# Kernel optimization log

Hardware: AMD Instinct MI355X
Metric: run time of the kernel (lower is better)

The kernel has to match this reference:

```python
import jax, jax.numpy as jnp
import numpy as np

B, S, D, H = 4, 2048, 1024, 16
HD = D // H  # 64


def setup_inputs() -> dict:
    key = jax.random.key(0)
    ks = jax.random.split(key, 9)
    s = 1.0 / np.sqrt(D)
    return {
        "x": jax.random.normal(ks[0], (B, S, D), dtype=jnp.float32),
        "Wq": jax.random.normal(ks[1], (D, D), dtype=jnp.float32) * s,
        "bq": jax.random.normal(ks[2], (D,), dtype=jnp.float32) * 0.01,
        "Wk": jax.random.normal(ks[3], (D, D), dtype=jnp.float32) * s,
        "bk": jax.random.normal(ks[4], (D,), dtype=jnp.float32) * 0.01,
        "Wv": jax.random.normal(ks[5], (D, D), dtype=jnp.float32) * s,
        "bv": jax.random.normal(ks[6], (D,), dtype=jnp.float32) * 0.01,
        "Wo": jax.random.normal(ks[7], (D, D), dtype=jnp.float32) * s,
        "bo": jax.random.normal(ks[8], (D,), dtype=jnp.float32) * 0.01,
    }


def reference(x, Wq, bq, Wk, bk, Wv, bv, Wo, bo):
    b, s, _ = x.shape
    # projections -> [b, h, s, hd]
    def proj(W, bias):
        return (x @ W.T + bias).reshape(b, s, H, HD).transpose(0, 2, 1, 3)
    q, k, v = proj(Wq, bq), proj(Wk, bk), proj(Wv, bv)
    # NOTE: source multiplies by sqrt(head_dim)**0.5 = head_dim**0.25 (quirk kept)
    scale = jnp.asarray(HD, dtype=x.dtype) ** 0.25
    scores = jnp.einsum("bhqd,bhkd->bhqk", q, k) * scale
    causal = jnp.tril(jnp.ones((s, s), dtype=bool))
    scores = jnp.where(causal, scores, -jnp.inf)
    attn = jax.nn.softmax(scores, axis=-1)  # dropout p=0 (eval) -> identity
    out = jnp.einsum("bhqk,bhkd->bhqd", attn, v)
    out = out.transpose(0, 2, 1, 3).reshape(b, s, D)
    return out @ Wo.T + bo
```

## Files before the change

### kernel.cpp

```cpp
#include <hip/hip_runtime.h>
#include <hip/hip_fp16.h>


typedef unsigned short u16;
typedef unsigned int u32;
typedef _Float16 half8 __attribute__((ext_vector_type(8)));
typedef float f32x4 __attribute__((ext_vector_type(4)));
typedef unsigned short ushort8 __attribute__((ext_vector_type(8)));
typedef unsigned short us4 __attribute__((ext_vector_type(4)));
typedef unsigned int u32x2 __attribute__((ext_vector_type(2)));

#define SCL2 4.0816663172343815f
#define SWZ(r) ((((r) ^ ((r) >> 3))) & 7)

__device__ __forceinline__ u16 f2h(float f) {
  return __half_as_ushort(__float2half(f));
}

__device__ __forceinline__ us4 pack4(float a, float b, float c, float d) {
  u32x2 t;
  t[0] = __builtin_bit_cast(u32, __builtin_amdgcn_cvt_pkrtz(a, b));
  t[1] = __builtin_bit_cast(u32, __builtin_amdgcn_cvt_pkrtz(c, d));
  return __builtin_bit_cast(us4, t);
}

__device__ __forceinline__ void gload16(const void* gsrc, void* ldst) {
  typedef __attribute__((address_space(1))) const void glob_t;
  typedef __attribute__((address_space(3))) void lds_t;
  __builtin_amdgcn_global_load_lds((glob_t*)gsrc, (lds_t*)ldst, 16, 0, 0);
}

__device__ __forceinline__ f32x4 mfma_f16(half8 a, half8 b, f32x4 c) {
  return __builtin_amdgcn_mfma_f32_16x16x32_f16(a, b, c, 0, 0, 0);
}

__global__ __launch_bounds__(256) void cvt_f32_f16(const float* __restrict__ in,
                                                   u16* __restrict__ out, int n8) {
  int i = blockIdx.x * 256 + threadIdx.x;
  if (i >= n8) return;
  const float4* p = (const float4*)in + (size_t)i * 2;
  float4 a = p[0], b = p[1];
  ushort8 v;
  v[0] = f2h(a.x); v[1] = f2h(a.y); v[2] = f2h(a.z); v[3] = f2h(a.w);
  v[4] = f2h(b.x); v[5] = f2h(b.y); v[6] = f2h(b.z); v[7] = f2h(b.w);
  *(ushort8*)(out + (size_t)i * 8) = v;
}

__device__ __forceinline__ void gemm_body(const u16* __restrict__ A, const u16* __restrict__ Bw,
                                          const float* __restrict__ bias,
                                          u16* __restrict__ Ch, float* __restrict__ Cf,
                                          u16* __restrict__ Vtp) {
  __shared__ __align__(16) u16 sA[128 * 32];
  __shared__ __align__(16) u16 sB[128 * 32];
  const int m0 = blockIdx.y * 128, n0 = blockIdx.x * 128;
  const int tid = threadIdx.x, w = tid >> 6, l = tid & 63;
  const int wm = (w >> 1) * 64, wn = (w & 1) * 64;
  f32x4 acc[4][4] = {};
  const int srow = tid >> 2, sch = (tid & 3) * 8;
  char* sAb = (char*)sA + w * 1024;
  char* sBb = (char*)sB + w * 1024;
  const u16* Ag0 = A + (size_t)(m0 + srow) * 1024 + sch;
  const u16* Ag1 = A + (size_t)(m0 + 64 + srow) * 1024 + sch;
  const u16* Bg0 = Bw + (size_t)(n0 + srow) * 1024 + sch;
  const u16* Bg1 = Bw + (size_t)(n0 + 64 + srow) * 1024 + sch;
  for (int kt = 0; kt < 32; ++kt) {
    const int k0 = kt * 32;
    __syncthreads();
    gload16(Ag0 + k0, sAb);
    gload16(Ag1 + k0, sAb + 4096);
    gload16(Bg0 + k0, sBb);
    gload16(Bg1 + k0, sBb + 4096);
    __syncthreads();
    half8 a[4], b[4];
#pragma unroll
    for (int mf = 0; mf < 4; ++mf)
      a[mf] = *(const half8*)&sA[(wm + mf * 16 + (l & 15)) * 32 + (l >> 4) * 8];
#pragma unroll
    for (int nf = 0; nf < 4; ++nf)
      b[nf] = *(const half8*)&sB[(wn + nf * 16 + (l & 15)) * 32 + (l >> 4) * 8];
#pragma unroll
    for (int mf = 0; mf < 4; ++mf)
#pragma unroll
      for (int nf = 0; nf < 4; ++nf)
        acc[mf][nf] = mfma_f16(a[mf], b[nf], acc[mf][nf]);
  }
  if (Vtp) {
#pragma unroll
    for (int nf = 0; nf < 4; ++nf) {
      const int col = n0 + wn + nf * 16 + (l & 15);
      const float bv = bias[col];
#pragma unroll
      for (int mf = 0; mf < 4; ++mf) {
        const int row = m0 + wm + mf * 16 + (l >> 4) * 4;
        us4 v;
#pragma unroll
        for (int r = 0; r < 4; ++r) v[r] = f2h(acc[mf][nf][r] + bv);
        *(us4*)(Vtp + (size_t)((row >> 11) * 16 + (col >> 6)) * 131072 +
                (size_t)(col & 63) * 2048 + (row & 2047)) = v;
      }
    }
  } else {
#pragma unroll
    for (int nf = 0; nf < 4; ++nf) {
      const int col = n0 + wn + nf * 16 + (l & 15);
      const float bv = bias[col];
#pragma unroll
      for (int mf = 0; mf < 4; ++mf) {
#pragma unroll
        for (int r = 0; r < 4; ++r) {
          const int row = m0 + wm + mf * 16 + (l >> 4) * 4 + r;
          float v = acc[mf][nf][r] + bv;
          if (Cf) Cf[(size_t)row * 1024 + col] = v;
          else    Ch[(size_t)row * 1024 + col] = f2h(v);
        }
      }
    }
  }
}

struct QkvArgs {
  const u16* B[3];
  const float* bias[3];
  u16* C[3];
};

__global__ __launch_bounds__(256) void gemm_qkv(const u16* __restrict__ A, QkvArgs ga) {
  const int z = blockIdx.z;
  if (z == 2) gemm_body(A, ga.B[2], ga.bias[2], nullptr, nullptr, ga.C[2]);
  else        gemm_body(A, ga.B[z], ga.bias[z], ga.C[z], nullptr, nullptr);
}

__global__ __launch_bounds__(256) void gemm_out(const u16* __restrict__ A, const u16* __restrict__ Bw,
                                                const float* __restrict__ bias, float* __restrict__ C) {
  gemm_body(A, Bw, bias, nullptr, C, nullptr);
}

__global__ __launch_bounds__(256) void attn_fused(const u16* __restrict__ Qb, const u16* __restrict__ Kb,
                                                  const u16* __restrict__ Vt, u16* __restrict__ Ob) {
  __shared__ __align__(16) u16 k_s[64 * 64];
  __shared__ __align__(16) u16 vt_s[64 * 64];
  __shared__ __align__(16) u16 p_s[4 * 16 * 64];
  const int bid = blockIdx.x;
  const int bh = bid & 63;
  const int pj = bid >> 6;
  const int b = bh >> 4, h = bh & 15;
  const size_t baseQ = (size_t)b * 2048 * 1024 + h * 64;
  const size_t baseV = (size_t)(b * 16 + h) * 131072;
  const int tid = threadIdx.x, w = tid >> 6, l = tid & 63;
  const int g = l >> 4, qi = l & 15;
  const int q_loc = w * 16 + qi;

  const int srow = w * 8 + (l >> 3);
  const int sch0 = (l & 7) ^ SWZ(srow);
  const int sch1 = (l & 7) ^ SWZ(srow + 32);
  char* kd0 = (char*)k_s + w * 1024;
  char* kd1 = (char*)k_s + 4096 + w * 1024;
  char* vd0 = (char*)vt_s + w * 1024;
  char* vd1 = (char*)vt_s + 4096 + w * 1024;
  int koff[4], pvoff[2];
#pragma unroll
  for (int nf = 0; nf < 4; ++nf) {
    const int row = nf * 16 + qi;
    koff[nf] = row * 64 + ((g ^ SWZ(row)) << 3);
  }
#pragma unroll
  for (int ks = 0; ks < 2; ++ks)
    pvoff[ks] = qi * 64 + (((ks * 4 + g) ^ SWZ(qi)) << 3);
  u16* pw = p_s + w * 1024;

  for (int half = 0; half < 2; ++half) {
    const int qt = half ? (31 - pj) : pj;
    const int q0 = qt * 64;
    const int q_glob = q0 + q_loc;

    half8 qf0, qf1;
    {
      const u16* qp = Qb + baseQ + (size_t)q_glob * 1024 + g * 8;
      qf0 = *(const half8*)(qp);
      qf1 = *(const half8*)(qp + 32);
    }
    const u16* pK0 = Kb + baseQ + (size_t)srow * 1024 + sch0 * 8;
    const u16* pK1 = Kb + baseQ + (size_t)(srow + 32) * 1024 + sch1 * 8;
    const u16* pV0 = Vt + baseV + (size_t)srow * 2048 + sch0 * 8;
    const u16* pV1 = Vt + baseV + (size_t)(srow + 32) * 2048 + sch1 * 8;

    f32x4 s[4], o[4] = {};
    float m_r = -INFINITY, l_r = 0.f;

    for (int kt = 0; kt <= qt; ++kt) {
      __syncthreads();
      gload16(pK0, kd0);
      gload16(pK1, kd1);
      gload16(pV0, vd0);
      gload16(pV1, vd1);
      pK0 += 65536; pK1 += 65536; pV0 += 64; pV1 += 64;
      __syncthreads();
#pragma unroll
      for (int nf = 0; nf < 4; ++nf) {
        half8 k0 = *(const half8*)(k_s + koff[nf]);
        half8 k1 = *(const half8*)(k_s + (koff[nf] ^ 32));
        f32x4 acc = {};
        acc = mfma_f16(k0, qf0, acc);
        acc = mfma_f16(k1, qf1, acc);
        s[nf] = acc * SCL2;
      }
      if (kt == qt) {
#pragma unroll
        for (int nf = 0; nf < 4; ++nf) {
          const int kb = nf * 16 + g * 4;
#pragma unroll
          for (int r = 0; r < 4; ++r)
            if (kb + r > q_loc) s[nf][r] = -INFINITY;
        }
      }
      float t = fmaxf(fmaxf(fmaxf(s[0][0], s[0][1]), s[0][2]),
                      fmaxf(fmaxf(s[0][3], s[1][0]), s[1][1]));
      t = fmaxf(t, fmaxf(fmaxf(s[1][2], s[1][3]), s[2][0]));
      t = fmaxf(t, fmaxf(fmaxf(s[2][1], s[2][2]), s[2][3]));
      t = fmaxf(t, fmaxf(fmaxf(s[3][0], s[3][1]), s[3][2]));
      t = fmaxf(t, s[3][3]);
      t = fmaxf(t, __shfl_xor(t, 16));
      t = fmaxf(t, __shfl_xor(t, 32));
      if (!__all(t <= m_r + 8.f)) {
        const float mn = fmaxf(m_r, t);
        const float al = __builtin_amdgcn_exp2f(m_r - mn);
        l_r *= al;
#pragma unroll
        for (int nf = 0; nf < 4; ++nf) o[nf] *= al;
        m_r = mn;
      }
      float rs = 0.f;
#pragma unroll
      for (int nf = 0; nf < 4; ++nf) {
#pragma unroll
        for (int r = 0; r < 4; ++r) {
          const float p = __builtin_amdgcn_exp2f(s[nf][r] - m_r);
          s[nf][r] = p;
          rs += p;
        }
      }
      rs += __shfl_xor(rs, 16);
      rs += __shfl_xor(rs, 32);
      l_r += rs;
#pragma unroll
      for (int nf = 0; nf < 4; ++nf) {
        const int c = nf * 2 + (g >> 1);
        *(us4*)(pw + qi * 64 + ((c ^ SWZ(qi)) << 3) + (g & 1) * 4) =
            pack4(s[nf][0], s[nf][1], s[nf][2], s[nf][3]);
      }
#pragma unroll
      for (int ks = 0; ks < 2; ++ks) {
        half8 pf = *(const half8*)(pw + pvoff[ks]);
#pragma unroll
        for (int nf = 0; nf < 4; ++nf) {
          const int vrow = nf * 16 + qi;
          half8 vf = *(const half8*)(vt_s + vrow * 64 + (((ks * 4 + g) ^ SWZ(vrow)) << 3));
          o[nf] = mfma_f16(vf, pf, o[nf]);
        }
      }
    }
    const float inv = 1.f / l_r;
    u16* op = Ob + (size_t)(b * 2048 + q_glob) * 1024 + h * 64 + g * 4;
#pragma unroll
    for (int nf = 0; nf < 4; ++nf)
      *(us4*)(op + nf * 16) =
          pack4(o[nf][0] * inv, o[nf][1] * inv, o[nf][2] * inv, o[nf][3] * inv);
  }
}

extern "C" void kernel_launch(void* const* d_in, const int* in_sizes, int n_in,
                              void* d_out, int out_size, void* d_ws, size_t ws_size,
                              hipStream_t stream) {
  (void)in_sizes; (void)n_in; (void)out_size; (void)ws_size;
  const float* x  = (const float*)d_in[0];
  const float* Wq = (const float*)d_in[1];
  const float* bq = (const float*)d_in[2];
  const float* Wk = (const float*)d_in[3];
  const float* bk = (const float*)d_in[4];
  const float* Wv = (const float*)d_in[5];
  const float* bv = (const float*)d_in[6];
  const float* Wo = (const float*)d_in[7];
  const float* bo = (const float*)d_in[8];

  u16* xb = (u16*)d_ws;
  u16* wq = xb + (size_t)8192 * 1024;
  u16* wk = wq + 1024 * 1024;
  u16* wv = wk + 1024 * 1024;
  u16* wo = wv + 1024 * 1024;
  u16* Qb = wo + 1024 * 1024;
  u16* Kb = Qb + (size_t)8192 * 1024;
  u16* Vt = Kb + (size_t)8192 * 1024;
  u16* Ab = xb;

  cvt_f32_f16<<<4096, 256, 0, stream>>>(x, xb, 1048576);
  cvt_f32_f16<<<512, 256, 0, stream>>>(Wq, wq, 131072);
  cvt_f32_f16<<<512, 256, 0, stream>>>(Wk, wk, 131072);
  cvt_f32_f16<<<512, 256, 0, stream>>>(Wv, wv, 131072);
  cvt_f32_f16<<<512, 256, 0, stream>>>(Wo, wo, 131072);

  QkvArgs ga;
  ga.B[0] = wq; ga.B[1] = wk; ga.B[2] = wv;
  ga.bias[0] = bq; ga.bias[1] = bk; ga.bias[2] = bv;
  ga.C[0] = Qb; ga.C[1] = Kb; ga.C[2] = Vt;
  gemm_qkv<<<dim3(8, 64, 3), 256, 0, stream>>>(xb, ga);

  attn_fused<<<1024, 256, 0, stream>>>(Qb, Kb, Vt, Ab);

  gemm_out<<<dim3(8, 64), 256, 0, stream>>>(Ab, wo, bo, (float*)d_out);
}
```

Before: 307.9 us.

## Double-buffer K/V tiles in shared memory for fused attention

The attention kernel now keeps two shared-memory buffers for K and V. It issues the global loads for the next key tile before computing on the current one, and needs only one barrier per iteration instead of two. Per-row V offsets are also precomputed into registers instead of being recomputed in the inner loop. The aim is to hide global-load latency behind the MFMA and softmax work. The cost is about twice the LDS for K and V, which may lower the number of blocks resident per CU.

```diff
diff --git a/kernel.cpp b/kernel.cpp
--- a/kernel.cpp
+++ b/kernel.cpp
@@ -137,8 +137,8 @@
 
 __global__ __launch_bounds__(256) void attn_fused(const u16* __restrict__ Qb, const u16* __restrict__ Kb,
                                                   const u16* __restrict__ Vt, u16* __restrict__ Ob) {
-  __shared__ __align__(16) u16 k_s[64 * 64];
-  __shared__ __align__(16) u16 vt_s[64 * 64];
+  __shared__ __align__(16) u16 k_s[2 * 64 * 64];
+  __shared__ __align__(16) u16 vt_s[2 * 64 * 64];
   __shared__ __align__(16) u16 p_s[4 * 16 * 64];
   const int bid = blockIdx.x;
   const int bh = bid & 63;
@@ -153,21 +153,35 @@
   const int srow = w * 8 + (l >> 3);
   const int sch0 = (l & 7) ^ SWZ(srow);
   const int sch1 = (l & 7) ^ SWZ(srow + 32);
-  char* kd0 = (char*)k_s + w * 1024;
-  char* kd1 = (char*)k_s + 4096 + w * 1024;
-  char* vd0 = (char*)vt_s + w * 1024;
-  char* vd1 = (char*)vt_s + 4096 + w * 1024;
-  int koff[4], pvoff[2];
+  int koff[4], pvoff[2], voff[4][2];
 #pragma unroll
   for (int nf = 0; nf < 4; ++nf) {
     const int row = nf * 16 + qi;
     koff[nf] = row * 64 + ((g ^ SWZ(row)) << 3);
+#pragma unroll
+    for (int ks = 0; ks < 2; ++ks)
+      voff[nf][ks] = row * 64 + (((ks * 4 + g) ^ SWZ(row)) << 3);
   }
 #pragma unroll
   for (int ks = 0; ks < 2; ++ks)
     pvoff[ks] = qi * 64 + (((ks * 4 + g) ^ SWZ(qi)) << 3);
   u16* pw = p_s + w * 1024;
 
+  const u16* pK0;
+  const u16* pK1;
+  const u16* pV0;
+  const u16* pV1;
+  auto stage = [&](int buf) {
+    char* kb = (char*)k_s + buf * 8192;
+    char* vb = (char*)vt_s + buf * 8192;
+    gload16(pK0, kb + w * 1024);
+    gload16(pK1, kb + 4096 + w * 1024);
+    gload16(pV0, vb + w * 1024);
+    gload16(pV1, vb + 4096 + w * 1024);
+    pK0 += 65536; pK1 += 65536; pV0 += 64; pV1 += 64;
+  };
+
+  int cur = 0;
   for (int half = 0; half < 2; ++half) {
     const int qt = half ? (31 - pj) : pj;
     const int q0 = qt * 64;
@@ -179,26 +193,25 @@
       qf0 = *(const half8*)(qp);
       qf1 = *(const half8*)(qp + 32);
     }
-    const u16* pK0 = Kb + baseQ + (size_t)srow * 1024 + sch0 * 8;
-    const u16* pK1 = Kb + baseQ + (size_t)(srow + 32) * 1024 + sch1 * 8;
-    const u16* pV0 = Vt + baseV + (size_t)srow * 2048 + sch0 * 8;
-    const u16* pV1 = Vt + baseV + (size_t)(srow + 32) * 2048 + sch1 * 8;
+    pK0 = Kb + baseQ + (size_t)srow * 1024 + sch0 * 8;
+    pK1 = Kb + baseQ + (size_t)(srow + 32) * 1024 + sch1 * 8;
+    pV0 = Vt + baseV + (size_t)srow * 2048 + sch0 * 8;
+    pV1 = Vt + baseV + (size_t)(srow + 32) * 2048 + sch1 * 8;
 
     f32x4 s[4], o[4] = {};
     float m_r = -INFINITY, l_r = 0.f;
 
+    stage(cur);
+    __syncthreads();
+
     for (int kt = 0; kt <= qt; ++kt) {
-      __syncthreads();
-      gload16(pK0, kd0);
-      gload16(pK1, kd1);
-      gload16(pV0, vd0);
-      gload16(pV1, vd1);
-      pK0 += 65536; pK1 += 65536; pV0 += 64; pV1 += 64;
-      __syncthreads();
+      if (kt < qt) stage(cur ^ 1);
+      const u16* kbuf = k_s + cur * 4096;
+      const u16* vbuf = vt_s + cur * 4096;
 #pragma unroll
       for (int nf = 0; nf < 4; ++nf) {
-        half8 k0 = *(const half8*)(k_s + koff[nf]);
-        half8 k1 = *(const half8*)(k_s + (koff[nf] ^ 32));
+        half8 k0 = *(const half8*)(kbuf + koff[nf]);
+        half8 k1 = *(const half8*)(kbuf + (koff[nf] ^ 32));
         f32x4 acc = {};
         acc = mfma_f16(k0, qf0, acc);
         acc = mfma_f16(k1, qf1, acc);
@@ -253,11 +266,12 @@
         half8 pf = *(const half8*)(pw + pvoff[ks]);
 #pragma unroll
         for (int nf = 0; nf < 4; ++nf) {
-          const int vrow = nf * 16 + qi;
-          half8 vf = *(const half8*)(vt_s + vrow * 64 + (((ks * 4 + g) ^ SWZ(vrow)) << 3));
+          half8 vf = *(const half8*)(vbuf + voff[nf][ks]);
           o[nf] = mfma_f16(vf, pf, o[nf]);
         }
       }
+      __syncthreads();
+      cur ^= 1;
     }
     const float inv = 1.f / l_r;
     u16* op = Ob + (size_t)(b * 2048 + q_glob) * 1024 + h * 64 + g * 4;
```

New measurement: 296.3 us. -3.8%, faster.
